# Performance work log

Hardware: AMD Instinct MI355X
Metric: run time of the kernel (lower is better)

Reference implementation:

```python
import jax, jax.numpy as jnp
from jax import lax
import numpy as np

V, E, H, B, S = 50000, 128, 64, 512, 512
OUT = 2


def _lstm_layer(x, Wih, Whh, bih, bhh):
    # x: [B, S, D]; Wih: [4H, D]; Whh: [4H, H]; PyTorch gate order i,f,g,o
    b = bih + bhh
    Bsz = x.shape[0]
    h0 = jnp.zeros((Bsz, H), x.dtype)
    c0 = jnp.zeros((Bsz, H), x.dtype)
    # precompute input projections for all timesteps (one big GEMM)
    xproj = jnp.einsum('bsd,gd->bsg', x, Wih) + b  # [B, S, 4H]

    def step(carry, xt):
        h, c = carry
        gates = xt + h @ Whh.T  # [B, 4H]
        i, f, g, o = jnp.split(gates, 4, axis=-1)
        i = jax.nn.sigmoid(i)
        f = jax.nn.sigmoid(f)
        g = jnp.tanh(g)
        o = jax.nn.sigmoid(o)
        c = f * c + i * g
        h = o * jnp.tanh(c)
        return (h, c), h

    (hT, cT), ys = lax.scan(step, (h0, c0), jnp.swapaxes(xproj, 0, 1))
    return jnp.swapaxes(ys, 0, 1), hT


def setup_inputs() -> dict:
    key = jax.random.key(0)
    ks = jax.random.split(key, 12)
    s = 0.05
    emb = jax.random.normal(ks[0], (V, E), jnp.float32) * s
    emb = emb.at[0].set(0.0)  # padding_idx=0
    inp = {
        'input_seq': jax.random.randint(ks[1], (B, S), 0, V, dtype=jnp.int64),
        'emb': emb,
        'Wih0': jax.random.normal(ks[2], (4 * H, E), jnp.float32) * s,
        'Whh0': jax.random.normal(ks[3], (4 * H, H), jnp.float32) * s,
        'bih0': jax.random.normal(ks[4], (4 * H,), jnp.float32) * s,
        'bhh0': jax.random.normal(ks[5], (4 * H,), jnp.float32) * s,
        'Wih1': jax.random.normal(ks[6], (4 * H, H), jnp.float32) * s,
        'Whh1': jax.random.normal(ks[7], (4 * H, H), jnp.float32) * s,
        'bih1': jax.random.normal(ks[8], (4 * H,), jnp.float32) * s,
        'bhh1': jax.random.normal(ks[9], (4 * H,), jnp.float32) * s,
        'Wfc': jax.random.normal(ks[10], (OUT, H), jnp.float32) * s,
        'bfc': jax.random.normal(ks[11], (OUT,), jnp.float32) * s,
    }
    return inp


def reference(input_seq, emb, Wih0, Whh0, bih0, bhh0, Wih1, Whh1, bih1, bhh1, Wfc, bfc):
    # eval-mode: dropouts are identity
    x = emb[input_seq]                       # [B, S, E] embedding lookup
    y0, h0T = _lstm_layer(x, Wih0, Whh0, bih0, bhh0)
    y1, h1T = _lstm_layer(y0, Wih1, Whh1, bih1, bhh1)
    out = jax.nn.sigmoid(h1T @ Wfc.T + bfc)  # [B, 2]
    return out
```

## Files before the change

### kernel.cpp

```cpp
#include <hip/hip_runtime.h>
#include <hip/hip_bf16.h>
#include <hip/hip_fp16.h>
#include <math.h>

#define Bv   512
#define Sv   512
#define Hv   64
#define Ev   128
#define G4   256
#define VV   50000
#define Rr   16

typedef _Float16 f16;
typedef _Float16 f16x2 __attribute__((ext_vector_type(2)));
typedef _Float16 f16x4 __attribute__((ext_vector_type(4)));
typedef _Float16 f16x8 __attribute__((ext_vector_type(8)));
typedef float    f32x4 __attribute__((ext_vector_type(4)));

#if __has_builtin(__builtin_amdgcn_exp2f)
#define EXP2F(x) __builtin_amdgcn_exp2f(x)
#else
#define EXP2F(x) exp2f(x)
#endif
#if __has_builtin(__builtin_amdgcn_rcpf)
#define RCPF(x) __builtin_amdgcn_rcpf(x)
#else
#define RCPF(x) (1.0f / (x))
#endif
#define LOG2E 1.442695040888963f

__device__ __forceinline__ float fast_sigmoid(float x) {
    float e = EXP2F(-LOG2E * x);
    return RCPF(1.0f + e);
}

__device__ __forceinline__ f16x2 PK(float a, float b) {
    return __builtin_bit_cast(f16x2, __builtin_amdgcn_cvt_pkrtz(a, b));
}
__device__ __forceinline__ f16x2 C2(float c) {
    f16 h = (f16)c;
    return f16x2{h, h};
}
__device__ __forceinline__ f16x2 clamp2(f16x2 x, f16x2 lo, f16x2 hi) {
    return __builtin_elementwise_min(__builtin_elementwise_max(x, lo), hi);
}
__device__ __forceinline__ f16x2 sig2(f16x2 x) {
    x = clamp2(x, C2(-2.f), C2(2.f));
    f16x2 x2 = x * x;
    f16x2 t = x2 * C2(-2.10813e-4f) + C2(2.08333333e-3f);
    t = x2 * t + C2(-2.08333333e-2f);
    t = x2 * t + C2(0.25f);
    return x * t + C2(0.5f);
}
__device__ __forceinline__ f16x2 tanh2(f16x2 x) {
    x = clamp2(x, C2(-1.f), C2(1.f));
    f16x2 x2 = x * x;
    f16x2 t = x2 * C2(-5.3968254e-2f) + C2(1.33333333e-1f);
    t = x2 * t + C2(-3.33333333e-1f);
    t = x2 * t + C2(1.f);
    return x * t;
}

__device__ __forceinline__ void cell_update4(const f32x4 acc[4], f16x2 c2[2],
                                             f16* dst, int stride) {
#pragma unroll
    for (int p = 0; p < 2; ++p) {
        f16x2 ig = sig2 (PK(acc[0][2 * p], acc[0][2 * p + 1]));
        f16x2 fg = sig2 (PK(acc[1][2 * p], acc[1][2 * p + 1]));
        f16x2 gg = tanh2(PK(acc[2][2 * p], acc[2][2 * p + 1]));
        f16x2 og = sig2 (PK(acc[3][2 * p], acc[3][2 * p + 1]));
        c2[p] = fg * c2[p] + ig * gg;
        f16x2 hv = og * tanh2(c2[p]);
        dst[(2 * p) * stride]     = hv[0];
        dst[(2 * p + 1) * stride] = hv[1];
    }
}

__global__ __launch_bounds__(256) void vocab_gemm_mfma(
    const float* __restrict__ emb,
    const float* __restrict__ Wih0,
    const float* __restrict__ bih0, const float* __restrict__ bhh0,
    f16* __restrict__ P2)
{
    const int tid  = threadIdx.x;
    const int w    = tid >> 6;
    const int lane = tid & 63;
    const int col  = lane & 15;
    const int quad = lane >> 4;
    const int u    = 16 * w + col;
    const size_t m0 = (size_t)blockIdx.x * 32;

    f16x8 Bf[4][4];
    float bb[4];
#pragma unroll
    for (int tt = 0; tt < 4; ++tt) {
        const int n = 64 * tt + u;
        const float* bp = Wih0 + (size_t)n * Ev + quad * 8;
#pragma unroll
        for (int kc = 0; kc < 4; ++kc) {
            f16x8 v;
#pragma unroll
            for (int j = 0; j < 8; ++j) v[j] = (f16)bp[kc * 32 + j];
            Bf[tt][kc] = v;
        }
        bb[tt] = bih0[n] + bhh0[n];
    }
    f16x8 Af[2][4];
#pragma unroll
    for (int mh = 0; mh < 2; ++mh) {
        size_t row = m0 + mh * 16 + col;
        if (row >= VV) row = 0;
        const float* ap = emb + row * (size_t)Ev + quad * 8;
#pragma unroll
        for (int kc = 0; kc < 4; ++kc) {
            f16x8 v;
#pragma unroll
            for (int j = 0; j < 8; ++j) v[j] = (f16)ap[kc * 32 + j];
            Af[mh][kc] = v;
        }
    }

    f32x4 acc[2][4];
#pragma unroll
    for (int mh = 0; mh < 2; ++mh)
#pragma unroll
        for (int tt = 0; tt < 4; ++tt) {
#pragma unroll
            for (int r = 0; r < 4; ++r) acc[mh][tt][r] = 0.f;
#pragma unroll
            for (int kc = 0; kc < 4; ++kc)
                acc[mh][tt] = __builtin_amdgcn_mfma_f32_16x16x32_f16(
                    Af[mh][kc], Bf[tt][kc], acc[mh][tt], 0, 0, 0);
        }

#pragma unroll
    for (int mh = 0; mh < 2; ++mh)
#pragma unroll
        for (int r = 0; r < 4; ++r) {
            size_t row = m0 + mh * 16 + quad * 4 + r;
            if (row < VV) {
                f16x4 pk;
#pragma unroll
                for (int tt = 0; tt < 4; ++tt)
                    pk[tt] = (f16)(acc[mh][tt][r] + bb[tt]);
                *(f16x4*)(P2 + row * (size_t)G4 + u * 4) = pk;
            }
        }
}

__device__ __forceinline__ void load_chunk(uint2 (&X)[4][4],
    const int (*idxl)[516], int rowbase, int sb, const f16* Pl2) {
    if (sb > Sv - 4) sb = Sv - 4;
#pragma unroll
    for (int r = 0; r < 4; ++r) {
        int4 v = *(const int4*)&idxl[rowbase + r][sb];
        X[r][0] = *(const uint2*)(Pl2 + (size_t)(unsigned)v.x * G4);
        X[r][1] = *(const uint2*)(Pl2 + (size_t)(unsigned)v.y * G4);
        X[r][2] = *(const uint2*)(Pl2 + (size_t)(unsigned)v.z * G4);
        X[r][3] = *(const uint2*)(Pl2 + (size_t)(unsigned)v.w * G4);
    }
}

__global__ __launch_bounds__(512) void lstm_mfma(
    const f16* __restrict__ P2,
    const int* __restrict__ idx,
    const float* __restrict__ Whh0,
    const float* __restrict__ Wih1,
    const float* __restrict__ Whh1,
    const float* __restrict__ bih1, const float* __restrict__ bhh1,
    const float* __restrict__ Wfc,
    const float* __restrict__ bfc,
    float* __restrict__ out)
{
    const int tid  = threadIdx.x;
    const int wave = tid >> 6;
    const int lane = tid & 63;
    const int grp  = wave >> 2;
    const int w    = wave & 3;
    const int col  = lane & 15;
    const int quad = lane >> 4;
    const int u    = 16 * w + col;
    const int rowbase = quad * 4;
    const int rb   = blockIdx.x * Rr;

    __shared__ __align__(16) f16 h0b[2][Rr][72];
    __shared__ __align__(16) f16 h1b[2][Rr][72];
    __shared__ __align__(16) int idxl[Rr][516];

    for (int k = tid; k < Rr * Sv; k += 512) {
        int r = k >> 9, s = k & 511;
        idxl[r][s] = idx[(size_t)(rb + r) * Sv + s];
    }
    for (int k = tid; k < 2 * Rr * 72; k += 512) {
        (&h0b[0][0][0])[k] = (f16)0.f;
        (&h1b[0][0][0])[k] = (f16)0.f;
    }

    f16x8 Bh[4][2];
    f16x8 Bi[4][2];
    f16x8 B1[4][2];
    float bg[4];
    if (grp == 0) {
#pragma unroll
        for (int g = 0; g < 4; ++g) {
            const int n = u + 64 * g;
#pragma unroll
            for (int kt = 0; kt < 2; ++kt) {
                const float* src = Whh0 + (size_t)n * Hv + kt * 32 + quad * 8;
                f16x8 v;
#pragma unroll
                for (int j = 0; j < 8; ++j) v[j] = (f16)src[j];
                Bh[g][kt] = v;
            }
            bg[g] = 0.f;
        }
    } else {
#pragma unroll
        for (int g = 0; g < 4; ++g) {
            const int n = u + 64 * g;
#pragma unroll
            for (int kt = 0; kt < 2; ++kt) {
                const float* si = Wih1 + (size_t)n * Hv + kt * 32 + quad * 8;
                const float* s1 = Whh1 + (size_t)n * Hv + kt * 32 + quad * 8;
                f16x8 vi, v1;
#pragma unroll
                for (int j = 0; j < 8; ++j) { vi[j] = (f16)si[j]; v1[j] = (f16)s1[j]; }
                Bi[g][kt] = vi;
                B1[g][kt] = v1;
            }
            bg[g] = bih1[n] + bhh1[n];
        }
    }

    f16x2 c2[2] = {C2(0.f), C2(0.f)};
    uint2 Xa[4][4], Xb[4][4];
    const f16* Pl2 = P2 + u * 4;

    __syncthreads();

    if (grp == 0) load_chunk(Xa, idxl, rowbase, 0, Pl2);

    for (int o = 0; o < Sv / 8; ++o) {
        const int s0 = o * 8;
#pragma unroll
        for (int j = 0; j < 8; ++j) {
            const int i = s0 + j;
            const int cur = j & 1, nxt = cur ^ 1;
            if (grp == 0) {
                f32x4 acc[4];
                {
                    const uint2 xw = (j < 4) ? Xa[0][j & 3] : Xb[0][j & 3];
                    (void)xw;
                }
#pragma unroll
                for (int r = 0; r < 4; ++r) {
                    f16x4 xf = __builtin_bit_cast(f16x4,
                        (j < 4) ? Xa[r][j & 3] : Xb[r][j & 3]);
#pragma unroll
                    for (int g = 0; g < 4; ++g) acc[g][r] = (float)xf[g];
                }
                if (j == 0) load_chunk(Xb, idxl, rowbase, s0 + 4, Pl2);
                if (j == 4) load_chunk(Xa, idxl, rowbase, s0 + 8, Pl2);
                f16x8 a0 = *(const f16x8*)&h0b[cur][col][quad * 8];
                f16x8 a1 = *(const f16x8*)&h0b[cur][col][32 + quad * 8];
#pragma unroll
                for (int g = 0; g < 4; ++g) {
                    acc[g] = __builtin_amdgcn_mfma_f32_16x16x32_f16(a0, Bh[g][0], acc[g], 0, 0, 0);
                    acc[g] = __builtin_amdgcn_mfma_f32_16x16x32_f16(a1, Bh[g][1], acc[g], 0, 0, 0);
                }
                cell_update4(acc, c2, &h0b[nxt][rowbase][u], 72);
            } else if (i >= 1) {
                f32x4 accA[4], accB[4];
                f16x8 a00 = *(const f16x8*)&h0b[cur][col][quad * 8];
                f16x8 a01 = *(const f16x8*)&h0b[cur][col][32 + quad * 8];
                f16x8 a10 = *(const f16x8*)&h1b[cur][col][quad * 8];
                f16x8 a11 = *(const f16x8*)&h1b[cur][col][32 + quad * 8];
#pragma unroll
                for (int g = 0; g < 4; ++g) {
#pragma unroll
                    for (int r = 0; r < 4; ++r) { accA[g][r] = bg[g]; accB[g][r] = 0.f; }
                    accA[g] = __builtin_amdgcn_mfma_f32_16x16x32_f16(a00, Bi[g][0], accA[g], 0, 0, 0);
                    accA[g] = __builtin_amdgcn_mfma_f32_16x16x32_f16(a01, Bi[g][1], accA[g], 0, 0, 0);
                    accB[g] = __builtin_amdgcn_mfma_f32_16x16x32_f16(a10, B1[g][0], accB[g], 0, 0, 0);
                    accB[g] = __builtin_amdgcn_mfma_f32_16x16x32_f16(a11, B1[g][1], accB[g], 0, 0, 0);
                }
                f32x4 acc[4];
#pragma unroll
                for (int g = 0; g < 4; ++g) acc[g] = accA[g] + accB[g];
                cell_update4(acc, c2, &h1b[nxt][rowbase][u], 72);
            }
            __syncthreads();
        }
    }

    if (grp == 1) {
        f32x4 acc[4];
#pragma unroll
        for (int g = 0; g < 4; ++g)
#pragma unroll
            for (int r = 0; r < 4; ++r) acc[g][r] = bg[g];
        f16x8 a00 = *(const f16x8*)&h0b[0][col][quad * 8];
        f16x8 a01 = *(const f16x8*)&h0b[0][col][32 + quad * 8];
        f16x8 a10 = *(const f16x8*)&h1b[0][col][quad * 8];
        f16x8 a11 = *(const f16x8*)&h1b[0][col][32 + quad * 8];
#pragma unroll
        for (int g = 0; g < 4; ++g) {
            acc[g] = __builtin_amdgcn_mfma_f32_16x16x32_f16(a00, Bi[g][0], acc[g], 0, 0, 0);
            acc[g] = __builtin_amdgcn_mfma_f32_16x16x32_f16(a01, Bi[g][1], acc[g], 0, 0, 0);
            acc[g] = __builtin_amdgcn_mfma_f32_16x16x32_f16(a10, B1[g][0], acc[g], 0, 0, 0);
            acc[g] = __builtin_amdgcn_mfma_f32_16x16x32_f16(a11, B1[g][1], acc[g], 0, 0, 0);
        }
        cell_update4(acc, c2, &h1b[1][rowbase][u], 72);
    }
    __syncthreads();

    if (tid < 2 * Rr) {
        const int r = tid >> 1, j = tid & 1;
        float s = bfc[j];
        const float* wf = Wfc + (size_t)j * Hv;
#pragma unroll 8
        for (int k = 0; k < Hv; ++k) s += (float)h1b[1][r][k] * wf[k];
        out[(size_t)(rb + r) * 2 + j] = fast_sigmoid(s);
    }
}

extern "C" void kernel_launch(void* const* d_in, const int* in_sizes, int n_in,
                              void* d_out, int out_size, void* d_ws, size_t ws_size,
                              hipStream_t stream)
{
    const int*   idx  = (const int*)  d_in[0];
    const float* emb  = (const float*)d_in[1];
    const float* Wih0 = (const float*)d_in[2];
    const float* Whh0 = (const float*)d_in[3];
    const float* bih0 = (const float*)d_in[4];
    const float* bhh0 = (const float*)d_in[5];
    const float* Wih1 = (const float*)d_in[6];
    const float* Whh1 = (const float*)d_in[7];
    const float* bih1 = (const float*)d_in[8];
    const float* bhh1 = (const float*)d_in[9];
    const float* Wfc  = (const float*)d_in[10];
    const float* bfc  = (const float*)d_in[11];
    float* out = (float*)d_out;

    f16* P2 = (f16*)d_ws;

    const int gemmBlocks = (VV + 31) / 32;
    vocab_gemm_mfma<<<gemmBlocks, 256, 0, stream>>>(emb, Wih0, bih0, bhh0, P2);
    lstm_mfma<<<Bv / Rr, 512, 0, stream>>>(P2, idx, Whh0,
                                           Wih1, Whh1, bih1, bhh1, Wfc, bfc, out);
}
```

Baseline: 464.6 us.

## Decouple LSTM layer wavefront groups with LDS counters and ring buffer

Replaces the per-timestep block-wide __syncthreads between the layer-0 and layer-1 wave groups with per-wave progress counters in shared memory and spin-waits. Layer-0 h states go into an 8-deep ring buffer, so layer 0 can run up to seven steps ahead of layer 1 instead of the two layers moving in lockstep. Weight loads also switch to float4 vectorized reads with packed conversion. Spin-waiting on volatile LDS costs issue slots and relies on fences for correctness, and the iteration cap on the spin loop could silently break ordering.

After: 580.1 us. +24.9%, slower.

```diff
diff --git a/kernel.cpp b/kernel.cpp
--- a/kernel.cpp
+++ b/kernel.cpp
@@ -73,6 +73,23 @@
         f16x2 hv = og * tanh2(c2[p]);
         dst[(2 * p) * stride]     = hv[0];
         dst[(2 * p + 1) * stride] = hv[1];
+    }
+}
+
+__device__ __forceinline__ f16x8 cvt8(float4 a, float4 b) {
+    f16x2 p0 = PK(a.x, a.y), p1 = PK(a.z, a.w);
+    f16x2 p2 = PK(b.x, b.y), p3 = PK(b.z, b.w);
+    f16x8 r;
+    r[0] = p0[0]; r[1] = p0[1]; r[2] = p1[0]; r[3] = p1[1];
+    r[4] = p2[0]; r[5] = p2[1]; r[6] = p3[0]; r[7] = p3[1];
+    return r;
+}
+
+__device__ __forceinline__ void spin_wait(volatile int* cnt, int need0, int need1) {
+    for (int it = 0; it < (1 << 20); ++it) {
+        int m0 = min(min(cnt[0], cnt[1]), min(cnt[2], cnt[3]));
+        int m1 = min(min(cnt[4], cnt[5]), min(cnt[6], cnt[7]));
+        if (m0 >= need0 && m1 >= need1) return;
     }
 }
 
@@ -95,13 +112,10 @@
 #pragma unroll
     for (int tt = 0; tt < 4; ++tt) {
         const int n = 64 * tt + u;
-        const float* bp = Wih0 + (size_t)n * Ev + quad * 8;
 #pragma unroll
         for (int kc = 0; kc < 4; ++kc) {
-            f16x8 v;
-#pragma unroll
-            for (int j = 0; j < 8; ++j) v[j] = (f16)bp[kc * 32 + j];
-            Bf[tt][kc] = v;
+            const float4* bp = (const float4*)(Wih0 + (size_t)n * Ev + kc * 32 + quad * 8);
+            Bf[tt][kc] = cvt8(bp[0], bp[1]);
         }
         bb[tt] = bih0[n] + bhh0[n];
     }
@@ -110,13 +124,10 @@
     for (int mh = 0; mh < 2; ++mh) {
         size_t row = m0 + mh * 16 + col;
         if (row >= VV) row = 0;
-        const float* ap = emb + row * (size_t)Ev + quad * 8;
 #pragma unroll
         for (int kc = 0; kc < 4; ++kc) {
-            f16x8 v;
-#pragma unroll
-            for (int j = 0; j < 8; ++j) v[j] = (f16)ap[kc * 32 + j];
-            Af[mh][kc] = v;
+            const float4* ap = (const float4*)(emb + row * (size_t)Ev + kc * 32 + quad * 8);
+            Af[mh][kc] = cvt8(ap[0], ap[1]);
         }
     }
 
@@ -183,36 +194,34 @@
     const int rowbase = quad * 4;
     const int rb   = blockIdx.x * Rr;
 
-    __shared__ __align__(16) f16 h0b[2][Rr][72];
+    __shared__ __align__(16) f16 h0r[8][Rr][72];
     __shared__ __align__(16) f16 h1b[2][Rr][72];
     __shared__ __align__(16) int idxl[Rr][516];
+    __shared__ int cnt[8];
+    volatile int* vc = cnt;
 
     for (int k = tid; k < Rr * Sv; k += 512) {
         int r = k >> 9, s = k & 511;
         idxl[r][s] = idx[(size_t)(rb + r) * Sv + s];
     }
-    for (int k = tid; k < 2 * Rr * 72; k += 512) {
-        (&h0b[0][0][0])[k] = (f16)0.f;
-        (&h1b[0][0][0])[k] = (f16)0.f;
-    }
+    for (int k = tid; k < 8 * Rr * 72; k += 512) (&h0r[0][0][0])[k] = (f16)0.f;
+    for (int k = tid; k < 2 * Rr * 72; k += 512) (&h1b[0][0][0])[k] = (f16)0.f;
+    if (tid < 8) cnt[tid] = 0;
 
     f16x8 Bh[4][2];
     f16x8 Bi[4][2];
     f16x8 B1[4][2];
-    float bg[4];
+    f32x4 bgv[4];
+    const f32x4 zero4 = {0.f, 0.f, 0.f, 0.f};
     if (grp == 0) {
 #pragma unroll
         for (int g = 0; g < 4; ++g) {
             const int n = u + 64 * g;
 #pragma unroll
             for (int kt = 0; kt < 2; ++kt) {
-                const float* src = Whh0 + (size_t)n * Hv + kt * 32 + quad * 8;
-                f16x8 v;
-#pragma unroll
-                for (int j = 0; j < 8; ++j) v[j] = (f16)src[j];
-                Bh[g][kt] = v;
-            }
-            bg[g] = 0.f;
+                const float4* sp = (const float4*)(Whh0 + (size_t)n * Hv + kt * 32 + quad * 8);
+                Bh[g][kt] = cvt8(sp[0], sp[1]);
+            }
         }
     } else {
 #pragma unroll
@@ -220,38 +229,32 @@
             const int n = u + 64 * g;
 #pragma unroll
             for (int kt = 0; kt < 2; ++kt) {
-                const float* si = Wih1 + (size_t)n * Hv + kt * 32 + quad * 8;
-                const float* s1 = Whh1 + (size_t)n * Hv + kt * 32 + quad * 8;
-                f16x8 vi, v1;
-#pragma unroll
-                for (int j = 0; j < 8; ++j) { vi[j] = (f16)si[j]; v1[j] = (f16)s1[j]; }
-                Bi[g][kt] = vi;
-                B1[g][kt] = v1;
-            }
-            bg[g] = bih1[n] + bhh1[n];
+                const float4* si = (const float4*)(Wih1 + (size_t)n * Hv + kt * 32 + quad * 8);
+                const float4* s1 = (const float4*)(Whh1 + (size_t)n * Hv + kt * 32 + quad * 8);
+                Bi[g][kt] = cvt8(si[0], si[1]);
+                B1[g][kt] = cvt8(s1[0], s1[1]);
+            }
+            float b = bih1[n] + bhh1[n];
+            bgv[g] = f32x4{b, b, b, b};
         }
     }
 
     f16x2 c2[2] = {C2(0.f), C2(0.f)};
-    uint2 Xa[4][4], Xb[4][4];
     const f16* Pl2 = P2 + u * 4;
 
     __syncthreads();
 
-    if (grp == 0) load_chunk(Xa, idxl, rowbase, 0, Pl2);
-
-    for (int o = 0; o < Sv / 8; ++o) {
-        const int s0 = o * 8;
-#pragma unroll
-        for (int j = 0; j < 8; ++j) {
-            const int i = s0 + j;
-            const int cur = j & 1, nxt = cur ^ 1;
-            if (grp == 0) {
+    if (grp == 0) {
+        uint2 Xa[4][4], Xb[4][4];
+        load_chunk(Xa, idxl, rowbase, 0, Pl2);
+        for (int o = 0; o < Sv / 8; ++o) {
+            const int s0 = o * 8;
+#pragma unroll
+            for (int j = 0; j < 8; ++j) {
+                const int s = s0 + j;
+                spin_wait(vc, s, s - 7);
+                __threadfence_block();
                 f32x4 acc[4];
-                {
-                    const uint2 xw = (j < 4) ? Xa[0][j & 3] : Xb[0][j & 3];
-                    (void)xw;
-                }
 #pragma unroll
                 for (int r = 0; r < 4; ++r) {
                     f16x4 xf = __builtin_bit_cast(f16x4,
@@ -261,57 +264,45 @@
                 }
                 if (j == 0) load_chunk(Xb, idxl, rowbase, s0 + 4, Pl2);
                 if (j == 4) load_chunk(Xa, idxl, rowbase, s0 + 8, Pl2);
-                f16x8 a0 = *(const f16x8*)&h0b[cur][col][quad * 8];
-                f16x8 a1 = *(const f16x8*)&h0b[cur][col][32 + quad * 8];
+                const int rp = (s - 1) & 7;
+                f16x8 a0 = *(const f16x8*)&h0r[rp][col][quad * 8];
+                f16x8 a1 = *(const f16x8*)&h0r[rp][col][32 + quad * 8];
 #pragma unroll
                 for (int g = 0; g < 4; ++g) {
                     acc[g] = __builtin_amdgcn_mfma_f32_16x16x32_f16(a0, Bh[g][0], acc[g], 0, 0, 0);
                     acc[g] = __builtin_amdgcn_mfma_f32_16x16x32_f16(a1, Bh[g][1], acc[g], 0, 0, 0);
                 }
-                cell_update4(acc, c2, &h0b[nxt][rowbase][u], 72);
-            } else if (i >= 1) {
-                f32x4 accA[4], accB[4];
-                f16x8 a00 = *(const f16x8*)&h0b[cur][col][quad * 8];
-                f16x8 a01 = *(const f16x8*)&h0b[cur][col][32 + quad * 8];
-                f16x8 a10 = *(const f16x8*)&h1b[cur][col][quad * 8];
-                f16x8 a11 = *(const f16x8*)&h1b[cur][col][32 + quad * 8];
-#pragma unroll
-                for (int g = 0; g < 4; ++g) {
-#pragma unroll
-                    for (int r = 0; r < 4; ++r) { accA[g][r] = bg[g]; accB[g][r] = 0.f; }
-                    accA[g] = __builtin_amdgcn_mfma_f32_16x16x32_f16(a00, Bi[g][0], accA[g], 0, 0, 0);
-                    accA[g] = __builtin_amdgcn_mfma_f32_16x16x32_f16(a01, Bi[g][1], accA[g], 0, 0, 0);
-                    accB[g] = __builtin_amdgcn_mfma_f32_16x16x32_f16(a10, B1[g][0], accB[g], 0, 0, 0);
-                    accB[g] = __builtin_amdgcn_mfma_f32_16x16x32_f16(a11, B1[g][1], accB[g], 0, 0, 0);
-                }
-                f32x4 acc[4];
-#pragma unroll
-                for (int g = 0; g < 4; ++g) acc[g] = accA[g] + accB[g];
-                cell_update4(acc, c2, &h1b[nxt][rowbase][u], 72);
-            }
-            __syncthreads();
-        }
-    }
-
-    if (grp == 1) {
-        f32x4 acc[4];
-#pragma unroll
-        for (int g = 0; g < 4; ++g)
-#pragma unroll
-            for (int r = 0; r < 4; ++r) acc[g][r] = bg[g];
-        f16x8 a00 = *(const f16x8*)&h0b[0][col][quad * 8];
-        f16x8 a01 = *(const f16x8*)&h0b[0][col][32 + quad * 8];
-        f16x8 a10 = *(const f16x8*)&h1b[0][col][quad * 8];
-        f16x8 a11 = *(const f16x8*)&h1b[0][col][32 + quad * 8];
-#pragma unroll
-        for (int g = 0; g < 4; ++g) {
-            acc[g] = __builtin_amdgcn_mfma_f32_16x16x32_f16(a00, Bi[g][0], acc[g], 0, 0, 0);
-            acc[g] = __builtin_amdgcn_mfma_f32_16x16x32_f16(a01, Bi[g][1], acc[g], 0, 0, 0);
-            acc[g] = __builtin_amdgcn_mfma_f32_16x16x32_f16(a10, B1[g][0], acc[g], 0, 0, 0);
-            acc[g] = __builtin_amdgcn_mfma_f32_16x16x32_f16(a11, B1[g][1], acc[g], 0, 0, 0);
-        }
-        cell_update4(acc, c2, &h1b[1][rowbase][u], 72);
-    }
+                cell_update4(acc, c2, &h0r[s & 7][rowbase][u], 72);
+                __threadfence_block();
+                if (lane == 0) vc[w] = s + 1;
+            }
+        }
+    } else {
+        for (int s = 0; s < Sv; ++s) {
+            spin_wait(vc, s + 1, s);
+            __threadfence_block();
+            const int rs = s & 7, hb = s & 1;
+            f16x8 a00 = *(const f16x8*)&h0r[rs][col][quad * 8];
+            f16x8 a01 = *(const f16x8*)&h0r[rs][col][32 + quad * 8];
+            f16x8 a10 = *(const f16x8*)&h1b[hb ^ 1][col][quad * 8];
+            f16x8 a11 = *(const f16x8*)&h1b[hb ^ 1][col][32 + quad * 8];
+            f32x4 accA[4], accB[4];
+#pragma unroll
+            for (int g = 0; g < 4; ++g) {
+                accA[g] = __builtin_amdgcn_mfma_f32_16x16x32_f16(a00, Bi[g][0], bgv[g], 0, 0, 0);
+                accA[g] = __builtin_amdgcn_mfma_f32_16x16x32_f16(a01, Bi[g][1], accA[g], 0, 0, 0);
+                accB[g] = __builtin_amdgcn_mfma_f32_16x16x32_f16(a10, B1[g][0], zero4, 0, 0, 0);
+                accB[g] = __builtin_amdgcn_mfma_f32_16x16x32_f16(a11, B1[g][1], accB[g], 0, 0, 0);
+            }
+            f32x4 acc[4];
+#pragma unroll
+            for (int g = 0; g < 4; ++g) acc[g] = accA[g] + accB[g];
+            cell_update4(acc, c2, &h1b[hb][rowbase][u], 72);
+            __threadfence_block();
+            if (lane == 0) vc[4 + w] = s + 1;
+        }
+    }
+
     __syncthreads();
 
     if (tid < 2 * Rr) {
```
